# Kernel optimization log

Measured on AMD Instinct MI355X. Metric: run time of the kernel, lower is better.

The kernel has to match this reference:

```python
import jax, jax.numpy as jnp
import numpy as np

NUM_RELS = 19


def rgcn_layer(h, W, b, src, dst, etype, n_nodes):
    """DGL RelGraphConv (basis regularizer, num_bases=num_rels, sum aggregation, bias, no self-loop).

    out[v] = sum_{e: dst(e)=v} W[etype(e)] @ h[src(e)] + b
    Computed as: aggregate h[src] per (relation, dst) pair, then one GEMM per relation.
    """
    # segment id combines relation and destination node -> [R*N] segments
    seg = etype * n_nodes + dst
    agg = jax.ops.segment_sum(h[src], seg, num_segments=NUM_RELS * n_nodes)
    agg = agg.reshape(NUM_RELS, n_nodes, h.shape[1])  # [R, N, in]
    return jnp.einsum('rni,rio->no', agg, W) + b       # [N, out]


def setup_inputs() -> dict:
    key = jax.random.key(0)
    ks = jax.random.split(key, 8)
    N, E, R, D = 100000, 1600000, NUM_RELS, 32
    s = 0.1  # keep activations well-scaled across layers
    return {
        'src': jax.random.randint(ks[0], (E,), 0, N, dtype=jnp.int32),
        'dst': jax.random.randint(ks[1], (E,), 0, N, dtype=jnp.int32),
        'etype': jax.random.randint(ks[2], (E,), 0, R, dtype=jnp.int32),
        'n_nodes': N,
        'W1': jax.random.normal(ks[3], (R, 1, D), jnp.float32) * s,
        'b1': jnp.zeros((D,), jnp.float32),
        'W2': jax.random.normal(ks[4], (R, D, D), jnp.float32) * s,
        'b2': jnp.zeros((D,), jnp.float32),
        'W3': jax.random.normal(ks[5], (D, D), jnp.float32) * s,
        'b3': jnp.zeros((D,), jnp.float32),
    }


def reference(src, dst, etype, n_nodes, W1, b1, W2, b2, W3, b3):
    # h = ones(N, 1), as in Embedder.forward
    h = jnp.ones((n_nodes, 1), jnp.float32)
    h = jax.nn.relu(rgcn_layer(h, W1, b1, src, dst, etype, n_nodes))
    h = jax.nn.relu(rgcn_layer(h, W2, b2, src, dst, etype, n_nodes))
    # conv_output=False -> final layer is a plain Linear
    return h @ W3 + b3
```

## Files before the change

### kernel.cpp

```cpp
#include <hip/hip_runtime.h>

#define NUM_RELS 19
#define NPB 256
#define NPB_SHIFT 8
#define MAXB 400
#define NBLK 512

typedef _Float16 half8 __attribute__((ext_vector_type(8)));
typedef float floatx4 __attribute__((ext_vector_type(4)));



__global__ void w2swz_kernel(const float* __restrict__ W2, _Float16* __restrict__ W2F,
                             int* __restrict__ bcnt, int B) {
    int idx = blockIdx.x * blockDim.x + threadIdx.x;
    if (idx < B) bcnt[idx] = 0;
    if (idx >= NUM_RELS * 2 * 64 * 8) return;
    int j = idx & 7, lane = (idx >> 3) & 63, nt = (idx >> 9) & 1, r = idx >> 10;
    int k = (lane >> 4) * 8 + j, n = nt * 16 + (lane & 15);
    W2F[idx] = (_Float16)W2[r * 1024 + k * 32 + n];
}


__global__ __launch_bounds__(512) void count_kernel(const int* __restrict__ dst,
                                                    int* __restrict__ blkhist,
                                                    int* __restrict__ bcnt,
                                                    int E, int B, int chunk) {
    __shared__ int h[MAXB];
    for (int i = threadIdx.x; i < B; i += 512) h[i] = 0;
    __syncthreads();
    int e0 = blockIdx.x * chunk, e1 = min(E, e0 + chunk);
    for (int e = e0 + (int)threadIdx.x; e < e1; e += 512)
        atomicAdd(&h[dst[e] >> NPB_SHIFT], 1);
    __syncthreads();
    for (int i = threadIdx.x; i < B; i += 512) {
        blkhist[blockIdx.x * B + i] = h[i];
        if (h[i]) atomicAdd(&bcnt[i], h[i]);
    }
}


__global__ __launch_bounds__(NBLK) void offscan_kernel(const int* __restrict__ blkhist,
                                                       const int* __restrict__ bcnt,
                                                       int* __restrict__ pbase,
                                                       int* __restrict__ offs, int B) {
    __shared__ int lds[NBLK];
    __shared__ int pbs;
    int bucket = blockIdx.x;
    int t = threadIdx.x;

    int c = (t < B) ? ((bcnt[t] + 7) & ~7) : 0;
    lds[t] = c;
    __syncthreads();
    for (int off = 1; off < NBLK; off <<= 1) {
        int x = (t >= off) ? lds[t - off] : 0;
        __syncthreads();
        lds[t] += x;
        __syncthreads();
    }
    if (t == bucket) {
        pbs = lds[t] - c;
        pbase[bucket] = pbs;
    }
    __syncthreads();
    int myp = pbs;

    int v = blkhist[t * B + bucket];
    lds[t] = v;
    __syncthreads();
    for (int off = 1; off < NBLK; off <<= 1) {
        int x = (t >= off) ? lds[t - off] : 0;
        __syncthreads();
        lds[t] += x;
        __syncthreads();
    }
    offs[t * B + bucket] = myp + lds[t] - v;
}


__global__ __launch_bounds__(512) void scatter2_kernel(
    const int* __restrict__ src, const int* __restrict__ dst, const int* __restrict__ etype,
    const int* __restrict__ offs, unsigned* __restrict__ recs4, int E, int B, int chunk) {
    __shared__ int cur[MAXB];
    for (int i = threadIdx.x; i < B; i += 512) cur[i] = offs[blockIdx.x * B + i];
    __syncthreads();
    int e0 = blockIdx.x * chunk, e1 = min(E, e0 + chunk);
    for (int e = e0 + (int)threadIdx.x; e < e1; e += 512) {
        int d = dst[e];
        int b = d >> NPB_SHIFT;
        int pos = atomicAdd(&cur[b], 1);
        recs4[pos] = ((unsigned)(d & (NPB - 1)) << 22) | ((unsigned)src[e] << 5) | (unsigned)etype[e];
    }
}


__global__ __launch_bounds__(512) void bsort_l1t_kernel(
    const unsigned* __restrict__ recs4, const int* __restrict__ pbase, const int* __restrict__ bcnt,
    int* __restrict__ recs2, int* __restrict__ row_start, int* __restrict__ rend,
    const float* __restrict__ W1, const float* __restrict__ b1,
    const _Float16* __restrict__ W2F, _Float16* __restrict__ g, int N) {
    __shared__ int hist[NPB];
    __shared__ int offsl[NPB];
    __shared__ int cur[NPB];
    __shared__ int cnt2[NPB * NUM_RELS];
    __shared__ float W1s[NUM_RELS * 32];
    __shared__ float b1s[32];
    __shared__ _Float16 h1t[NPB * 32];
    int b = blockIdx.x;
    int p0 = pbase[b], n = bcnt[b];
    int t = threadIdx.x;

    if (t < NPB) hist[t] = 0;
    for (int i = t; i < NPB * NUM_RELS; i += 512) cnt2[i] = 0;
    for (int i = t; i < NUM_RELS * 32; i += 512) W1s[i] = W1[i];
    if (t < 32) b1s[t] = b1[t];
    __syncthreads();

    for (int i = t; i < n; i += 512) {
        unsigned rec = recs4[p0 + i];
        int ln = rec >> 22;
        atomicAdd(&hist[ln], 1);
        atomicAdd(&cnt2[ln * NUM_RELS + (rec & 31)], 1);
    }
    __syncthreads();
    int c = 0;
    if (t < NPB) {
        c = hist[t];
        offsl[t] = c;
    }
    __syncthreads();
    for (int off = 1; off < NPB; off <<= 1) {
        int x = 0;
        if (t < NPB && t >= off) x = offsl[t - off];
        __syncthreads();
        if (t < NPB) offsl[t] += x;
        __syncthreads();
    }
    if (t < NPB) {
        int start = p0 + offsl[t] - c;
        cur[t] = start;
        int v = (b << NPB_SHIFT) + t;
        if (v < N) {
            row_start[v] = start;
            rend[v] = start + c;
        }
    }
    __syncthreads();
    for (int i = t; i < n; i += 512) {
        unsigned rec = recs4[p0 + i];
        int p = atomicAdd(&cur[rec >> 22], 1);
        recs2[p] = (int)(rec & 0x3FFFFFu);
    }

    int o = t & 31, hw = t >> 5;
    int v0n = b << NPB_SHIFT;
    for (int k = hw; k < NPB; k += 16) {
        int vv = v0n + k;
        float acc = b1s[o];
        const int* cp = &cnt2[k * NUM_RELS];
#pragma unroll
        for (int r = 0; r < NUM_RELS; ++r) acc += (float)cp[r] * W1s[r * 32 + o];
        h1t[k * 32 + o] = (vv < N) ? (_Float16)fmaxf(acc, 0.f) : (_Float16)0.f;
    }
    __syncthreads();

    int lane = t & 63;
    int wv = t >> 6;
    floatx4 zero = {0.f, 0.f, 0.f, 0.f};
    int row = (lane >> 4) * 4;
    int col = lane & 15;
    for (int tile = wv; tile < NPB / 16; tile += 8) {
        int v0g = v0n + tile * 16;
        if (v0g >= N) continue;
        half8 a = *(const half8*)(h1t + (tile * 16 + (lane & 15)) * 32 + (lane >> 4) * 8);
        for (int r = 0; r < NUM_RELS; ++r) {
            _Float16* gbase = g + ((size_t)r * N + v0g) * 32;
#pragma unroll
            for (int nt = 0; nt < 2; ++nt) {
                half8 bfrag = *(const half8*)(W2F + ((r * 2 + nt) * 64 + lane) * 8);
                floatx4 d = __builtin_amdgcn_mfma_f32_16x16x32_f16(a, bfrag, zero, 0, 0, 0);
#pragma unroll
                for (int reg = 0; reg < 4; ++reg) {
                    gbase[(row + reg) * 32 + nt * 16 + col] = (_Float16)d[reg];
                }
            }
        }
    }
}


__global__ __launch_bounds__(512) void edge23_kernel(
    const _Float16* __restrict__ g, const int* __restrict__ row_start,
    const int* __restrict__ rend, const int* __restrict__ recs2,
    const float* __restrict__ b2, const float* __restrict__ W3, const float* __restrict__ b3,
    float* __restrict__ out, int N) {
    __shared__ float W3s[1024];
    __shared__ float b2s[32], b3s[32];
    for (int i = threadIdx.x; i < 1024; i += 512) W3s[i] = W3[i];
    if (threadIdx.x < 32) {
        b2s[threadIdx.x] = b2[threadIdx.x];
        b3s[threadIdx.x] = b3[threadIdx.x];
    }
    __syncthreads();

    int o = threadIdx.x & 31;
    int hw = blockIdx.x * 16 + (threadIdx.x >> 5);
    if (hw >= N) return;
    int start = row_start[hw], end = rend[hw];
    const int sN32 = N * 32;

    float acc = b2s[o];
    for (int base = start; base < end; base += 32) {
        int idx = base + o;
        int m_l = (idx < end) ? recs2[idx] : 0;
        int cnt = min(32, end - base);
        int j = 0;
        for (; j + 4 <= cnt; j += 4) {
            float x[4];
#pragma unroll
            for (int k = 0; k < 4; ++k) {
                int m = __shfl(m_l, j + k, 32);
                x[k] = (float)g[(m & 31) * sN32 + (m >> 5) * 32 + o];
            }
            acc += ((x[0] + x[1]) + (x[2] + x[3]));
        }
        for (; j < cnt; ++j) {
            int m = __shfl(m_l, j, 32);
            acc += (float)g[(m & 31) * sN32 + (m >> 5) * 32 + o];
        }
    }
    float h2v = fmaxf(acc, 0.f);

    float acc3 = b3s[o];
#pragma unroll
    for (int i = 0; i < 32; ++i) {
        float hi = __shfl(h2v, i, 32);
        acc3 = fmaf(hi, W3s[i * 32 + o], acc3);
    }
    out[(size_t)hw * 32 + o] = acc3;
}


extern "C" void kernel_launch(void* const* d_in, const int* in_sizes, int n_in,
                              void* d_out, int out_size, void* d_ws, size_t ws_size,
                              hipStream_t stream) {
    const int* src   = (const int*)d_in[0];
    const int* dst   = (const int*)d_in[1];
    const int* etype = (const int*)d_in[2];
    const float* W1  = (const float*)d_in[4];
    const float* b1  = (const float*)d_in[5];
    const float* W2  = (const float*)d_in[6];
    const float* b2  = (const float*)d_in[7];
    const float* W3  = (const float*)d_in[8];
    const float* b3  = (const float*)d_in[9];
    float* out = (float*)d_out;

    int E = in_sizes[0];
    int N = out_size / 32;
    int B = (N + NPB - 1) >> NPB_SHIFT;

    char* ws = (char*)d_ws;
    size_t off = 0;
    auto alloc = [&](size_t bytes) {
        void* p = ws + off;
        off = (off + bytes + 255) & ~(size_t)255;
        return p;
    };
    int* bcnt       = (int*)alloc((size_t)MAXB * 4);
    int* pbase      = (int*)alloc((size_t)MAXB * 4);
    int* blkhist    = (int*)alloc((size_t)NBLK * MAXB * 4);
    int* offs       = (int*)alloc((size_t)NBLK * MAXB * 4);
    int* row_start  = (int*)alloc((size_t)N * 4);
    int* rend       = (int*)alloc((size_t)N * 4);
    unsigned* recs4 = (unsigned*)alloc(((size_t)E + 8 * MAXB + 64) * 4);
    int* recs2      = (int*)alloc(((size_t)E + 8 * MAXB + 64) * 4);
    _Float16* g     = (_Float16*)alloc((size_t)NUM_RELS * N * 32 * 2);
    _Float16* W2F   = (_Float16*)alloc((size_t)NUM_RELS * 2 * 64 * 8 * 2);

    w2swz_kernel<<<(NUM_RELS * 2 * 64 * 8 + 255) / 256, 256, 0, stream>>>(W2, W2F, bcnt, B);

    int chunk = (E + NBLK - 1) / NBLK;
    count_kernel<<<NBLK, 512, 0, stream>>>(dst, blkhist, bcnt, E, B, chunk);
    offscan_kernel<<<B, NBLK, 0, stream>>>(blkhist, bcnt, pbase, offs, B);
    scatter2_kernel<<<NBLK, 512, 0, stream>>>(src, dst, etype, offs, recs4, E, B, chunk);

    bsort_l1t_kernel<<<B, 512, 0, stream>>>(recs4, pbase, bcnt, recs2, row_start, rend,
                                            W1, b1, W2F, g, N);

    edge23_kernel<<<(N + 15) / 16, 512, 0, stream>>>(g, row_start, rend, recs2, b2, W3, b3, out, N);
}
```

Measured before the change: 210.0 us.

## Aggregate layer-2 inputs per relation before GEMM instead of pre-transforming all nodes

The code no longer precomputes h1 @ W2[r] for every node and relation, which meant writing and then gathering a 19xNx32 fp16 tensor. Layer-1 output h1 is now stored compactly, and edges are sorted by (dst, relation) inside each bucket. The edge kernel then sums h1[src] per relation run into shared memory and applies the 19 W2 matrices with MFMA per 16-node tile. This cuts global memory traffic and the gather footprint a lot. In exchange it adds shared-memory aggregation, a branchy per-relation accumulation loop, and only 2 of 8 waves doing the MFMA work.

```diff
diff --git a/kernel.cpp b/kernel.cpp
--- a/kernel.cpp
+++ b/kernel.cpp
@@ -94,18 +94,16 @@
 }
 
 
-__global__ __launch_bounds__(512) void bsort_l1t_kernel(
+__global__ __launch_bounds__(512) void bsort_l1_kernel(
     const unsigned* __restrict__ recs4, const int* __restrict__ pbase, const int* __restrict__ bcnt,
     int* __restrict__ recs2, int* __restrict__ row_start, int* __restrict__ rend,
     const float* __restrict__ W1, const float* __restrict__ b1,
-    const _Float16* __restrict__ W2F, _Float16* __restrict__ g, int N) {
+    _Float16* __restrict__ h1, int N) {
     __shared__ int hist[NPB];
     __shared__ int offsl[NPB];
-    __shared__ int cur[NPB];
     __shared__ int cnt2[NPB * NUM_RELS];
     __shared__ float W1s[NUM_RELS * 32];
     __shared__ float b1s[32];
-    __shared__ _Float16 h1t[NPB * 32];
     int b = blockIdx.x;
     int p0 = pbase[b], n = bcnt[b];
     int t = threadIdx.x;
@@ -136,108 +134,128 @@
         if (t < NPB) offsl[t] += x;
         __syncthreads();
     }
+    int v0n = b << NPB_SHIFT;
     if (t < NPB) {
         int start = p0 + offsl[t] - c;
-        cur[t] = start;
-        int v = (b << NPB_SHIFT) + t;
+        int v = v0n + t;
         if (v < N) {
             row_start[v] = start;
             rend[v] = start + c;
         }
     }
     __syncthreads();
+
+    int o = t & 31, hw = t >> 5;
+    for (int k = hw; k < NPB; k += 16) {
+        int vv = v0n + k;
+        if (vv < N) {
+            float acc = b1s[o];
+            const int* cp = &cnt2[k * NUM_RELS];
+#pragma unroll
+            for (int r = 0; r < NUM_RELS; ++r) acc += (float)cp[r] * W1s[r * 32 + o];
+            h1[(size_t)vv * 32 + o] = (_Float16)fmaxf(acc, 0.f);
+        }
+    }
+    __syncthreads();
+
+    if (t < NPB) {
+        int base = p0 + offsl[t] - c;
+        for (int r = 0; r < NUM_RELS; ++r) {
+            int cv = cnt2[t * NUM_RELS + r];
+            cnt2[t * NUM_RELS + r] = base;
+            base += cv;
+        }
+    }
+    __syncthreads();
+
     for (int i = t; i < n; i += 512) {
         unsigned rec = recs4[p0 + i];
-        int p = atomicAdd(&cur[rec >> 22], 1);
+        int p = atomicAdd(&cnt2[(rec >> 22) * NUM_RELS + (rec & 31)], 1);
         recs2[p] = (int)(rec & 0x3FFFFFu);
     }
-
-    int o = t & 31, hw = t >> 5;
-    int v0n = b << NPB_SHIFT;
-    for (int k = hw; k < NPB; k += 16) {
-        int vv = v0n + k;
-        float acc = b1s[o];
-        const int* cp = &cnt2[k * NUM_RELS];
-#pragma unroll
-        for (int r = 0; r < NUM_RELS; ++r) acc += (float)cp[r] * W1s[r * 32 + o];
-        h1t[k * 32 + o] = (vv < N) ? (_Float16)fmaxf(acc, 0.f) : (_Float16)0.f;
+}
+
+
+#define AGG_STRIDE (NUM_RELS * 32 + 4)
+
+__global__ __launch_bounds__(512) void edge23_kernel(
+    const _Float16* __restrict__ h1, const int* __restrict__ row_start,
+    const int* __restrict__ rend, const int* __restrict__ recs2,
+    const _Float16* __restrict__ W2F,
+    const float* __restrict__ b2, const float* __restrict__ W3, const float* __restrict__ b3,
+    float* __restrict__ out, int N) {
+    __shared__ float agg[16 * AGG_STRIDE];
+    __shared__ float h2t[16 * 32];
+    __shared__ float W3s[1024];
+    __shared__ float b2s[32], b3s[32];
+    int t = threadIdx.x;
+    for (int i = t; i < 16 * AGG_STRIDE; i += 512) agg[i] = 0.f;
+    for (int i = t; i < 1024; i += 512) W3s[i] = W3[i];
+    if (t < 32) {
+        b2s[t] = b2[t];
+        b3s[t] = b3[t];
+    }
+    __syncthreads();
+
+    int o = t & 31;
+    int hw = t >> 5;
+    int node = blockIdx.x * 16 + hw;
+    if (node < N) {
+        int start = row_start[node], end = rend[node];
+        float acc = 0.f;
+        int cur_r = -1;
+        float* aggn = agg + hw * AGG_STRIDE;
+        for (int base = start; base < end; base += 32) {
+            int idx = base + o;
+            int m_l = (idx < end) ? recs2[idx] : 0;
+            int cnt = min(32, end - base);
+            for (int j = 0; j < cnt; ++j) {
+                int m = __shfl(m_l, j, 32);
+                int r = m & 31;
+                if (r != cur_r) {
+                    if (cur_r >= 0) aggn[cur_r * 32 + o] = acc;
+                    acc = 0.f;
+                    cur_r = r;
+                }
+                acc += (float)h1[(size_t)(m >> 5) * 32 + o];
+            }
+        }
+        if (cur_r >= 0) aggn[cur_r * 32 + o] = acc;
     }
     __syncthreads();
 
     int lane = t & 63;
     int wv = t >> 6;
-    floatx4 zero = {0.f, 0.f, 0.f, 0.f};
-    int row = (lane >> 4) * 4;
-    int col = lane & 15;
-    for (int tile = wv; tile < NPB / 16; tile += 8) {
-        int v0g = v0n + tile * 16;
-        if (v0g >= N) continue;
-        half8 a = *(const half8*)(h1t + (tile * 16 + (lane & 15)) * 32 + (lane >> 4) * 8);
+    if (wv < 2) {
+        int nt = wv;
+        floatx4 accd = {0.f, 0.f, 0.f, 0.f};
+        const float* ap0 = agg + (lane & 15) * AGG_STRIDE + (lane >> 4) * 8;
         for (int r = 0; r < NUM_RELS; ++r) {
-            _Float16* gbase = g + ((size_t)r * N + v0g) * 32;
+            const float* ap = ap0 + r * 32;
+            half8 a;
 #pragma unroll
-            for (int nt = 0; nt < 2; ++nt) {
-                half8 bfrag = *(const half8*)(W2F + ((r * 2 + nt) * 64 + lane) * 8);
-                floatx4 d = __builtin_amdgcn_mfma_f32_16x16x32_f16(a, bfrag, zero, 0, 0, 0);
+            for (int j = 0; j < 8; ++j) a[j] = (_Float16)ap[j];
+            half8 bfrag = *(const half8*)(W2F + ((r * 2 + nt) * 64 + lane) * 8);
+            accd = __builtin_amdgcn_mfma_f32_16x16x32_f16(a, bfrag, accd, 0, 0, 0);
+        }
+        int col = lane & 15, rowb = (lane >> 4) * 4;
 #pragma unroll
-                for (int reg = 0; reg < 4; ++reg) {
-                    gbase[(row + reg) * 32 + nt * 16 + col] = (_Float16)d[reg];
-                }
-            }
-        }
-    }
-}
-
-
-__global__ __launch_bounds__(512) void edge23_kernel(
-    const _Float16* __restrict__ g, const int* __restrict__ row_start,
-    const int* __restrict__ rend, const int* __restrict__ recs2,
-    const float* __restrict__ b2, const float* __restrict__ W3, const float* __restrict__ b3,
-    float* __restrict__ out, int N) {
-    __shared__ float W3s[1024];
-    __shared__ float b2s[32], b3s[32];
-    for (int i = threadIdx.x; i < 1024; i += 512) W3s[i] = W3[i];
-    if (threadIdx.x < 32) {
-        b2s[threadIdx.x] = b2[threadIdx.x];
-        b3s[threadIdx.x] = b3[threadIdx.x];
-    }
-    __syncthreads();
-
-    int o = threadIdx.x & 31;
-    int hw = blockIdx.x * 16 + (threadIdx.x >> 5);
-    if (hw >= N) return;
-    int start = row_start[hw], end = rend[hw];
-    const int sN32 = N * 32;
-
-    float acc = b2s[o];
-    for (int base = start; base < end; base += 32) {
-        int idx = base + o;
-        int m_l = (idx < end) ? recs2[idx] : 0;
-        int cnt = min(32, end - base);
-        int j = 0;
-        for (; j + 4 <= cnt; j += 4) {
-            float x[4];
+        for (int reg = 0; reg < 4; ++reg) {
+            h2t[(rowb + reg) * 32 + nt * 16 + col] = fmaxf(accd[reg] + b2s[nt * 16 + col], 0.f);
+        }
+    }
+    __syncthreads();
+
+    if (node < N) {
+        float h2v = h2t[hw * 32 + o];
+        float acc3 = b3s[o];
 #pragma unroll
-            for (int k = 0; k < 4; ++k) {
-                int m = __shfl(m_l, j + k, 32);
-                x[k] = (float)g[(m & 31) * sN32 + (m >> 5) * 32 + o];
-            }
-            acc += ((x[0] + x[1]) + (x[2] + x[3]));
-        }
-        for (; j < cnt; ++j) {
-            int m = __shfl(m_l, j, 32);
-            acc += (float)g[(m & 31) * sN32 + (m >> 5) * 32 + o];
-        }
-    }
-    float h2v = fmaxf(acc, 0.f);
-
-    float acc3 = b3s[o];
-#pragma unroll
-    for (int i = 0; i < 32; ++i) {
-        float hi = __shfl(h2v, i, 32);
-        acc3 = fmaf(hi, W3s[i * 32 + o], acc3);
-    }
-    out[(size_t)hw * 32 + o] = acc3;
+        for (int i = 0; i < 32; ++i) {
+            float hi = __shfl(h2v, i, 32);
+            acc3 = fmaf(hi, W3s[i * 32 + o], acc3);
+        }
+        out[(size_t)node * 32 + o] = acc3;
+    }
 }
 
 
@@ -274,7 +292,7 @@
     int* rend       = (int*)alloc((size_t)N * 4);
     unsigned* recs4 = (unsigned*)alloc(((size_t)E + 8 * MAXB + 64) * 4);
     int* recs2      = (int*)alloc(((size_t)E + 8 * MAXB + 64) * 4);
-    _Float16* g     = (_Float16*)alloc((size_t)NUM_RELS * N * 32 * 2);
+    _Float16* h1    = (_Float16*)alloc(((size_t)N + NPB) * 32 * 2);
     _Float16* W2F   = (_Float16*)alloc((size_t)NUM_RELS * 2 * 64 * 8 * 2);
 
     w2swz_kernel<<<(NUM_RELS * 2 * 64 * 8 + 255) / 256, 256, 0, stream>>>(W2, W2F, bcnt, B);
@@ -284,8 +302,9 @@
     offscan_kernel<<<B, NBLK, 0, stream>>>(blkhist, bcnt, pbase, offs, B);
     scatter2_kernel<<<NBLK, 512, 0, stream>>>(src, dst, etype, offs, recs4, E, B, chunk);
 
-    bsort_l1t_kernel<<<B, 512, 0, stream>>>(recs4, pbase, bcnt, recs2, row_start, rend,
-                                            W1, b1, W2F, g, N);
-
-    edge23_kernel<<<(N + 15) / 16, 512, 0, stream>>>(g, row_start, rend, recs2, b2, W3, b3, out, N);
-}
+    bsort_l1_kernel<<<B, 512, 0, stream>>>(recs4, pbase, bcnt, recs2, row_start, rend,
+                                           W1, b1, h1, N);
+
+    edge23_kernel<<<(N + 15) / 16, 512, 0, stream>>>(h1, row_start, rend, recs2, W2F,
+                                                     b2, W3, b3, out, N);
+}
```

After: 310.2 us. 47.8% more time.
